# Performance work log

Measured on AMD Instinct MI355X. Metric: run time of the kernel, lower is better.

## Reference

```python
import jax, jax.numpy as jnp
import numpy as np

E, B, T, DIN, D = 8, 16, 512, 256, 256  # ensemble, batch, seq, input_dim, d_model*factor


def setup_inputs() -> dict:
    key = jax.random.key(0)
    ks = jax.random.split(key, 9)
    s_in = 1.0 / np.sqrt(DIN)
    s_d = 1.0 / np.sqrt(D)
    return {
        "x": jax.random.normal(ks[0], (E, B, T, DIN), jnp.float32),
        "hidden": jnp.zeros((1, E * B, 2 * D), jnp.float32),
        "rnn_start": (jax.random.uniform(ks[1], (B, T, 1)) < 0.02).astype(jnp.float32),
        "W_in": jax.random.normal(ks[2], (2, E, DIN, D), jnp.float32) * s_in,
        "b_in": jax.random.normal(ks[3], (2, E, D), jnp.float32) * 0.01,
        "W_mid": jax.random.normal(ks[4], (4, E, D, D), jnp.float32) * s_d,
        "b_mid": jax.random.normal(ks[5], (4, E, D), jnp.float32) * 0.01,
        "W_out": jax.random.normal(ks[6], (E, D, D), jnp.float32) * s_d,
        "b_out": jax.random.normal(ks[7], (E, D), jnp.float32) * 0.01,
    }


def _scan_tie_input_gate(v, f, h0):
    # h_t = f_t * h_{t-1} + (1 - f_t) * v_t  (tied input gate), via associative scan.
    # v, f: [N, T, D]; h0: [N, 1, D]
    b = (1.0 - f) * v

    def combine(x, y):
        a1, b1 = x
        a2, b2 = y
        return a1 * a2, a2 * b1 + b2

    A, Bc = jax.lax.associative_scan(combine, (f, b), axis=1)
    out = A * h0 + Bc  # [N, T, D]
    return out, out[:, -1:, :]


def reference(x, hidden, rnn_start, W_in, b_in, W_mid, b_mid, W_out, b_out):
    # --- first GILR stage ---
    u = jnp.einsum('ebti,meio->mebto', x, W_in) + b_in[:, :, None, None, :]
    v = jnp.tanh(u[0])
    f = jax.nn.sigmoid(u[1])
    f = f * (1.0 - rnn_start)[None]  # rnn_start [B,T,1] broadcasts over E, D

    vr = v.reshape(E * B, T, D)
    fr = f.reshape(E * B, T, D)

    h_pre, h_mid = jnp.split(hidden, 2, axis=-1)          # each [1, E*B, D]
    h_pre = jnp.transpose(h_pre, (1, 0, 2))               # [E*B, 1, D]
    h_mid = jnp.transpose(h_mid, (1, 0, 2))

    vr, h_pre_last = _scan_tie_input_gate(vr, fr, h_pre)
    v4 = vr.reshape(E, B, T, D)

    # --- LSTM-like middle stage ---
    u = jnp.einsum('ebti,meio->mebto', v4, W_mid) + b_mid[:, :, None, None, :]
    f = jax.nn.sigmoid(u[0])
    i = jax.nn.sigmoid(u[1])
    o = jax.nn.sigmoid(u[2])
    z = jnp.tanh(u[3])
    f = f * (1.0 - rnn_start)[None]

    fr = f.reshape(E * B, T, D)
    izr = (i * z).reshape(E * B, T, D)
    orr = o.reshape(E * B, T, D)

    out, h_mid_last = _scan_tie_input_gate(izr, fr, h_mid)
    out = out * orr
    out4 = out.reshape(E, B, T, D)

    # --- output projection ---
    out4 = jnp.einsum('ebti,eio->ebto', out4, W_out) + b_out[:, None, None, :]

    hidden_out = jnp.transpose(jnp.concatenate([h_pre_last, h_mid_last], axis=-1), (1, 0, 2))
    return out4, hidden_out
```

## Files before the change

kernel.cpp:

```cpp
#include <hip/hip_runtime.h>
#include <hip/hip_bf16.h>
#include <stdint.h>
#include <stddef.h>


typedef __bf16 bf16x8 __attribute__((ext_vector_type(8)));
typedef __bf16 bf16x4 __attribute__((ext_vector_type(4)));
typedef __bf16 bf16x2 __attribute__((ext_vector_type(2)));
typedef float  f32x4  __attribute__((ext_vector_type(4)));
typedef float  f32x2  __attribute__((ext_vector_type(2)));

#define E_ 8
#define M_ 8192
#define K_ 256

__device__ __forceinline__ float sigm_f(float x) {
    return __builtin_amdgcn_rcpf(1.0f + __expf(-x));
}
__device__ __forceinline__ float tanh_f(float x) {
    return 1.0f - 2.0f * __builtin_amdgcn_rcpf(1.0f + __expf(2.0f * x));
}

__device__ __forceinline__ void g2lds16(const void* g, void* l) {
    __builtin_amdgcn_global_load_lds((const __attribute__((address_space(1))) void*)g,
                                     (__attribute__((address_space(3))) void*)l, 16, 0, 0);
}

template <int D>
__device__ __forceinline__ float dppshr(float x) {
    return __builtin_bit_cast(float,
        __builtin_amdgcn_update_dpp(0, __builtin_bit_cast(int, x),
                                    0x110 | D, 0xF, 0xF, true));
}

__device__ __forceinline__ void lane_scan(float& A, float& B, float& EA, float& EB, int ln15) {
    float As, Bs;
    Bs = dppshr<1>(B); As = dppshr<1>(A); B = __builtin_fmaf(A, Bs, B); A = (ln15 >= 1) ? A * As : A;
    Bs = dppshr<2>(B); As = dppshr<2>(A); B = __builtin_fmaf(A, Bs, B); A = (ln15 >= 2) ? A * As : A;
    Bs = dppshr<4>(B); As = dppshr<4>(A); B = __builtin_fmaf(A, Bs, B); A = (ln15 >= 4) ? A * As : A;
    Bs = dppshr<8>(B); As = dppshr<8>(A); B = __builtin_fmaf(A, Bs, B); A = (ln15 >= 8) ? A * As : A;
    EA = dppshr<1>(A); EA = (ln15 >= 1) ? EA : 1.0f;
    EB = dppshr<1>(B);
}

__global__ __launch_bounds__(256) void convx_k(const float* __restrict__ x, __bf16* __restrict__ xb) {
    int i = blockIdx.x * 256 + threadIdx.x;
    float4 v = ((const float4*)x)[i];
    bf16x4 o;
    o[0] = (__bf16)v.x; o[1] = (__bf16)v.y; o[2] = (__bf16)v.z; o[3] = (__bf16)v.w;
    ((bf16x4*)xb)[i] = o;
}

__global__ __launch_bounds__(256) void transw_k(const float* __restrict__ src, __bf16* __restrict__ dst,
                                                int NG, int ilv) {
    int ge = blockIdx.z;
    int g = ge >> 3, e = ge & 7;
    int k0 = blockIdx.x * 64, d0 = blockIdx.y * 64;
    __shared__ float tile[64][65];
    int t = threadIdx.x;
#pragma unroll
    for (int j = 0; j < 16; ++j) {
        int lin = j * 256 + t;
        int r = lin >> 6, c = lin & 63;
        tile[r][c] = src[((size_t)(ge * 256 + k0 + r)) * 256 + d0 + c];
    }
    __syncthreads();
#pragma unroll
    for (int j = 0; j < 16; ++j) {
        int lin = j * 256 + t;
        int r = lin >> 6, c = lin & 63;
        int d = d0 + r;
        int row = ilv ? (d * NG + g) : (g * 256 + d);
        dst[((size_t)(e * NG * 256 + row)) * K_ + k0 + c] = (__bf16)tile[c][r];
    }
}

template <int MODE, int NG>
__global__ __launch_bounds__(512, 1) void gemm_k(const __bf16* __restrict__ A,
                                                 const __bf16* __restrict__ Wt,
                                                 const float* __restrict__ bias,
                                                 const float* __restrict__ rs,
                                                 __bf16* __restrict__ gout,
                                                 float* __restrict__ fout,
                                                 const float* __restrict__ hidden,
                                                 float* __restrict__ hidout) {
    constexpr int NT  = NG * 2;
    constexpr int NMT = 2 * NT;
    const int tid = threadIdx.x;
    const int bid = blockIdx.x;
    const int e  = bid & 7;
    const int rr = bid >> 3;
    const int nt = rr & (NT - 1);
    const int ms = rr / NT;
    const int mt0 = ms * NMT;
    const int lane = tid & 63, wid = tid >> 6;
    const int wr = wid >> 2, wc = wid & 3;
    const int ln15 = lane & 15, ln16 = lane >> 4;

    __shared__ __align__(16) __bf16 As[2][32768];
    __shared__ float cAl[64], cBl[64];
    __shared__ float chL[2][64];

    bf16x8 Breg[2][8];
    {
        const __bf16* bp = Wt + ((size_t)e * (NG * 256) + nt * 128 + wc * 32 + ln15) * K_ + ln16 * 8;
#pragma unroll
        for (int j = 0; j < 2; ++j)
#pragma unroll
            for (int s = 0; s < 8; ++s)
                Breg[j][s] = *(const bf16x8*)(bp + (size_t)j * 16 * K_ + s * 32);
    }
    f32x4 bias_v[2];
#pragma unroll
    for (int j = 0; j < 2; ++j) {
        int n0 = nt * 128 + wc * 32 + j * 16 + (ln16 << 2);
        if constexpr (MODE == 0) {
#pragma unroll
            for (int q = 0; q < 4; ++q) {
                int n = n0 + q;
                bias_v[j][q] = bias[((n & 1) * E_ + e) * 256 + (n >> 1)];
            }
        } else if constexpr (MODE == 1) {
#pragma unroll
            for (int q = 0; q < 4; ++q) {
                int n = n0 + q;
                bias_v[j][q] = bias[((n & 3) * E_ + e) * 256 + (n >> 2)];
            }
        } else {
            bias_v[j] = *(const f32x4*)&bias[e * 256 + n0];
        }
    }

    const size_t Ae = ((size_t)e * M_ + (size_t)mt0 * 128) * K_;
    const int sr = tid >> 5, sr2 = sr >> 2;
    const int gg0 = (tid & 31) ^ sr2;
    const __bf16* sE = A + Ae + (size_t)sr * K_ + gg0 * 8;
    const __bf16* sO = A + Ae + (size_t)sr * K_ + (gg0 ^ 4) * 8;
    __bf16* const dbase0 = &As[0][tid * 8];
    __bf16* const dbase1 = &As[1][tid * 8];

    auto stage = [&](int tt, int buf) {
        __bf16* d = buf ? dbase1 : dbase0;
        const size_t toff = (size_t)tt * (128 * K_);
#pragma unroll
        for (int q = 0; q < 8; ++q)
            g2lds16(((q & 1) ? sO : sE) + toff + q * (16 * K_), d + q * 4096);
    };

    const int rowb = (wr * 64 + ln15 * 4) * K_;
    const int gb = ln16 ^ (lane & 7);
    const int pe_off = rowb + gb * 8;
    const int po_off = rowb + (gb ^ 4) * 8;

    auto compute = [&](f32x4 (&acc)[4][2], int buf) {
        const __bf16* pe = &As[0][0] + buf * 32768 + pe_off;
        const __bf16* po = &As[0][0] + buf * 32768 + po_off;
#pragma unroll
        for (int s = 0; s < 8; ++s) {
            const __bf16* p = (s & 1) ? po : pe;
            bf16x8 af[4];
#pragma unroll
            for (int i = 0; i < 4; ++i)
                af[i] = *(const bf16x8*)(p + i * K_ + (s >> 1) * 64);
#pragma unroll
            for (int i = 0; i < 4; ++i)
#pragma unroll
                for (int j = 0; j < 2; ++j)
                    acc[i][j] = __builtin_amdgcn_mfma_f32_16x16x32_bf16(Breg[j][s], af[i], acc[i][j], 0, 0, 0);
        }
    };

    stage(0, 0);
    asm volatile("s_waitcnt vmcnt(0)" ::: "memory");
    __builtin_amdgcn_s_barrier();
    __builtin_amdgcn_sched_barrier(0);

    if constexpr (MODE == 2) {
        f32x4 acc[4][2] = {};
        int buf = 0;
        for (int t = 0; t < NMT; ++t) {
            if (t + 1 < NMT) stage(t + 1, buf ^ 1);
            compute(acc, buf);
            const int mb = (mt0 + t) * 128 + wr * 64 + ln15 * 4;
#pragma unroll
            for (int j = 0; j < 2; ++j) {
                const int n0 = nt * 128 + wc * 32 + j * 16 + (ln16 << 2);
#pragma unroll
                for (int i = 0; i < 4; ++i) {
                    f32x4 o = acc[i][j] + bias_v[j];
                    *(f32x4*)&fout[((size_t)e * M_ + mb + i) * 256 + n0] = o;
                    acc[i][j] = f32x4{};
                }
            }
            asm volatile("s_waitcnt vmcnt(8) lgkmcnt(0)" ::: "memory");
            __builtin_amdgcn_s_barrier();
            __builtin_amdgcn_sched_barrier(0);
            buf ^= 1;
        }
        return;
    } else {
        auto do_epi = [&](f32x4 (&acc)[4][2], int tp, const f32x4& rs4p, const float* hidvp) {
            const bool cs = ((tp & 3) == 0);
            const int c = tp >> 2;
            const int mb = (mt0 + tp) * 128 + wr * 64 + ln15 * 4;
            f32x4 rsv;
#pragma unroll
            for (int q = 0; q < 4; ++q) rsv[q] = 1.0f - rs4p[q];

            if constexpr (MODE == 1) {
                float PA[2][4], PB[2][4], Ov[2][4], LA[2], LB[2], EA[2], EB[2];
#pragma unroll
                for (int j = 0; j < 2; ++j) {
#pragma unroll
                    for (int i = 0; i < 4; ++i) {
                        float f  = sigm_f(acc[i][j][0] + bias_v[j][0]) * rsv[i];
                        float iv = sigm_f(acc[i][j][1] + bias_v[j][1]);
                        float o  = sigm_f(acc[i][j][2] + bias_v[j][2]);
                        float z  = tanh_f(acc[i][j][3] + bias_v[j][3]);
                        float b  = (1.0f - f) * iv * z;
                        Ov[j][i] = o;
                        if (i == 0) { PA[j][0] = f; PB[j][0] = b; }
                        else { PB[j][i] = __builtin_fmaf(f, PB[j][i - 1], b); PA[j][i] = PA[j][i - 1] * f; }
                        acc[i][j] = f32x4{};
                    }
                    LA[j] = PA[j][3]; LB[j] = PB[j][3];
                    lane_scan(LA[j], LB[j], EA[j], EB[j], ln15);
                }
                if (wr == 0 && ln15 == 15) {
#pragma unroll
                    for (int j = 0; j < 2; ++j) {
                        int sl = wc * 8 + j * 4 + ln16;
                        cAl[sl] = LA[j]; cBl[sl] = LB[j];
                    }
                }
                asm volatile("s_waitcnt lgkmcnt(0)" ::: "memory");
                __builtin_amdgcn_s_barrier();
#pragma unroll
                for (int j = 0; j < 2; ++j) {
                    const int sl = wc * 8 + j * 4 + ln16;
                    const int d = nt * 32 + wc * 8 + j * 4 + ln16;
                    float hp = cs ? hidvp[j] : chL[tp & 1][sl];
                    float hs = wr ? __builtin_fmaf(cAl[sl], hp, cBl[sl]) : hp;
                    float h0 = __builtin_fmaf(EA[j], hs, EB[j]);
#pragma unroll
                    for (int i = 0; i < 4; ++i) {
                        float h = __builtin_fmaf(PA[j][i], h0, PB[j][i]);
                        gout[((size_t)e * M_ + mb + i) * 256 + d] = (__bf16)(h * Ov[j][i]);
                    }
                    if (wr == 1 && ln15 == 15) {
                        float he = __builtin_fmaf(LA[j], hs, LB[j]);
                        chL[(tp + 1) & 1][sl] = he;
                        if ((tp & 3) == 3)
                            hidout[(e * 16 + ms * 4 + c) * 512 + 256 + d] = he;
                    }
                }
            } else {
                float PA[2][2][4], PB[2][2][4], LA[2][2], LB[2][2], EA[2][2], EB[2][2];
#pragma unroll
                for (int j = 0; j < 2; ++j) {
#pragma unroll
                    for (int dq = 0; dq < 2; ++dq) {
#pragma unroll
                        for (int i = 0; i < 4; ++i) {
                            float uv = acc[i][j][dq * 2 + 0] + bias_v[j][dq * 2 + 0];
                            float uf = acc[i][j][dq * 2 + 1] + bias_v[j][dq * 2 + 1];
                            float f = sigm_f(uf) * rsv[i];
                            float b = (1.0f - f) * tanh_f(uv);
                            if (i == 0) { PA[j][dq][0] = f; PB[j][dq][0] = b; }
                            else { PB[j][dq][i] = __builtin_fmaf(f, PB[j][dq][i - 1], b);
                                   PA[j][dq][i] = PA[j][dq][i - 1] * f; }
                        }
                        LA[j][dq] = PA[j][dq][3]; LB[j][dq] = PB[j][dq][3];
                        lane_scan(LA[j][dq], LB[j][dq], EA[j][dq], EB[j][dq], ln15);
                    }
#pragma unroll
                    for (int i = 0; i < 4; ++i) acc[i][j] = f32x4{};
                }
                if (wr == 0 && ln15 == 15) {
#pragma unroll
                    for (int j = 0; j < 2; ++j)
#pragma unroll
                        for (int dq = 0; dq < 2; ++dq) {
                            int sl = wc * 16 + j * 8 + ln16 * 2 + dq;
                            cAl[sl] = LA[j][dq]; cBl[sl] = LB[j][dq];
                        }
                }
                asm volatile("s_waitcnt lgkmcnt(0)" ::: "memory");
                __builtin_amdgcn_s_barrier();
#pragma unroll
                for (int j = 0; j < 2; ++j) {
                    const int D0 = nt * 64 + wc * 16 + j * 8 + ln16 * 2;
                    float h0q[2];
#pragma unroll
                    for (int dq = 0; dq < 2; ++dq) {
                        const int sl = wc * 16 + j * 8 + ln16 * 2 + dq;
                        float hp = cs ? hidvp[j * 2 + dq] : chL[tp & 1][sl];
                        float hs = wr ? __builtin_fmaf(cAl[sl], hp, cBl[sl]) : hp;
                        h0q[dq] = __builtin_fmaf(EA[j][dq], hs, EB[j][dq]);
                        if (wr == 1 && ln15 == 15) {
                            float he = __builtin_fmaf(LA[j][dq], hs, LB[j][dq]);
                            chL[(tp + 1) & 1][sl] = he;
                            if ((tp & 3) == 3)
                                hidout[(e * 16 + ms * 2 + c) * 512 + D0 + dq] = he;
                        }
                    }
#pragma unroll
                    for (int i = 0; i < 4; ++i) {
                        float ha = __builtin_fmaf(PA[j][0][i], h0q[0], PB[j][0][i]);
                        float hb = __builtin_fmaf(PA[j][1][i], h0q[1], PB[j][1][i]);
                        bf16x2 pk; pk[0] = (__bf16)ha; pk[1] = (__bf16)hb;
                        *(unsigned int*)&gout[((size_t)e * M_ + mb + i) * 256 + D0] =
                            __builtin_bit_cast(unsigned int, pk);
                    }
                }
            }
        };

        f32x4 accA[4][2] = {}, accB[4][2] = {};
        f32x4 rs4_p = {};
        float hidv_p[4] = {0.f, 0.f, 0.f, 0.f};
        int buf = 0;

        auto iter = [&](int t, f32x4 (&accC)[4][2], f32x4 (&accP)[4][2]) {
            const int c = t >> 2;
            f32x4 rs4_n;
            float hidv_n[4] = {0.f, 0.f, 0.f, 0.f};
            {
                const int mbh = (mt0 + t) * 128 + wr * 64 + ln15 * 4;
                rs4_n = *(const f32x4*)&rs[mbh];
                if constexpr (MODE == 1) {
                    const int nrow = e * 16 + ms * 4 + c;
                    hidv_n[0] = hidden[nrow * 512 + 256 + (nt * 32 + wc * 8 + 0 + ln16)];
                    hidv_n[1] = hidden[nrow * 512 + 256 + (nt * 32 + wc * 8 + 4 + ln16)];
                } else {
                    const int nrow = e * 16 + ms * 2 + c;
                    f32x2 ha = *(const f32x2*)&hidden[nrow * 512 + (nt * 64 + wc * 16 + 0 + ln16 * 2)];
                    f32x2 hb = *(const f32x2*)&hidden[nrow * 512 + (nt * 64 + wc * 16 + 8 + ln16 * 2)];
                    hidv_n[0] = ha[0]; hidv_n[1] = ha[1]; hidv_n[2] = hb[0]; hidv_n[3] = hb[1];
                }
                __builtin_amdgcn_sched_barrier(0);
            }
            if (t + 1 < NMT) stage(t + 1, buf ^ 1);
            compute(accC, buf);
            if (t > 0) do_epi(accP, t - 1, rs4_p, hidv_p);
            if (t == 0) {
                asm volatile("s_waitcnt vmcnt(0) lgkmcnt(0)" ::: "memory");
            } else {
                asm volatile("s_waitcnt vmcnt(8) lgkmcnt(0)" ::: "memory");
            }
            __builtin_amdgcn_s_barrier();
            __builtin_amdgcn_sched_barrier(0);
            buf ^= 1;
            rs4_p = rs4_n;
#pragma unroll
            for (int q = 0; q < 4; ++q) hidv_p[q] = hidv_n[q];
        };

#pragma unroll 1
        for (int t2 = 0; t2 < NMT; t2 += 2) {
            iter(t2, accA, accB);
            iter(t2 + 1, accB, accA);
        }
        do_epi(accB, NMT - 1, rs4_p, hidv_p);
    }
}

extern "C" void kernel_launch(void* const* d_in, const int* in_sizes, int n_in,
                              void* d_out, int out_size, void* d_ws, size_t ws_size,
                              hipStream_t stream) {
    const float* x      = (const float*)d_in[0];
    const float* hidden = (const float*)d_in[1];
    const float* rs     = (const float*)d_in[2];
    const float* W_in   = (const float*)d_in[3];
    const float* b_in   = (const float*)d_in[4];
    const float* W_mid  = (const float*)d_in[5];
    const float* b_mid  = (const float*)d_in[6];
    const float* W_out  = (const float*)d_in[7];
    const float* b_out  = (const float*)d_in[8];
    float* out = (float*)d_out;

    char* ws = (char*)d_ws;
    const size_t MiB = (size_t)1 << 20;
    __bf16* Wt1 = (__bf16*)(ws + 0);
    __bf16* Wt2 = (__bf16*)(ws + 2 * MiB);
    __bf16* Wt3 = (__bf16*)(ws + 6 * MiB);
    __bf16* v4b = (__bf16*)(ws + 8 * MiB);
    __bf16* xb  = (__bf16*)(ws + 40 * MiB);
    __bf16* G   = (__bf16*)(ws + 72 * MiB);

    float* hidout = out + (size_t)E_ * M_ * 256;

    convx_k<<<16384, 256, 0, stream>>>(x, xb);
    transw_k<<<dim3(4, 4, 16), 256, 0, stream>>>(W_in, Wt1, 2, 1);
    transw_k<<<dim3(4, 4, 32), 256, 0, stream>>>(W_mid, Wt2, 4, 1);
    transw_k<<<dim3(4, 4, 8), 256, 0, stream>>>(W_out, Wt3, 1, 0);

    gemm_k<0, 2><<<256, 512, 0, stream>>>(xb, Wt1, b_in, rs, v4b, nullptr, hidden, hidout);
    gemm_k<1, 4><<<256, 512, 0, stream>>>(v4b, Wt2, b_mid, rs, G, nullptr, hidden, hidout);
    gemm_k<2, 1><<<256, 512, 0, stream>>>(G, Wt3, b_out, nullptr, nullptr, out, nullptr, nullptr);
}
```

Baseline: 170.9 us.

## Fuse fp32-to-bf16 input conversion into first GEMM and merge weight transposes

Drops the standalone convx_k kernel. The first GEMM now loads fp32 x directly into registers, converts it to bf16, and writes it to LDS in a register-staged software pipeline. This removes the bf16 copy of x (a 32 MiB write plus its reread) and one launch. It also folds the three weight-transpose launches into a single launch. The cost is higher register pressure and twice the global bytes per tile in MODE 0, and the LDS write now happens after the wait for global loads rather than asynchronously.

```diff
diff --git a/kernel.cpp b/kernel.cpp
--- a/kernel.cpp
+++ b/kernel.cpp
@@ -43,17 +43,17 @@
     EB = dppshr<1>(B);
 }
 
-__global__ __launch_bounds__(256) void convx_k(const float* __restrict__ x, __bf16* __restrict__ xb) {
-    int i = blockIdx.x * 256 + threadIdx.x;
-    float4 v = ((const float4*)x)[i];
-    bf16x4 o;
-    o[0] = (__bf16)v.x; o[1] = (__bf16)v.y; o[2] = (__bf16)v.z; o[3] = (__bf16)v.w;
-    ((bf16x4*)xb)[i] = o;
-}
-
-__global__ __launch_bounds__(256) void transw_k(const float* __restrict__ src, __bf16* __restrict__ dst,
-                                                int NG, int ilv) {
-    int ge = blockIdx.z;
+__global__ __launch_bounds__(256) void transw_all(const float* __restrict__ W_in,
+                                                  const float* __restrict__ W_mid,
+                                                  const float* __restrict__ W_out,
+                                                  __bf16* __restrict__ Wt1,
+                                                  __bf16* __restrict__ Wt2,
+                                                  __bf16* __restrict__ Wt3) {
+    int z = blockIdx.z;
+    const float* src; __bf16* dst; int NG, ilv, ge;
+    if (z < 16)      { src = W_in;  dst = Wt1; NG = 2; ilv = 1; ge = z; }
+    else if (z < 48) { src = W_mid; dst = Wt2; NG = 4; ilv = 1; ge = z - 16; }
+    else             { src = W_out; dst = Wt3; NG = 1; ilv = 0; ge = z - 48; }
     int g = ge >> 3, e = ge & 7;
     int k0 = blockIdx.x * 64, d0 = blockIdx.y * 64;
     __shared__ float tile[64][65];
@@ -77,6 +77,7 @@
 
 template <int MODE, int NG>
 __global__ __launch_bounds__(512, 1) void gemm_k(const __bf16* __restrict__ A,
+                                                 const float* __restrict__ Af,
                                                  const __bf16* __restrict__ Wt,
                                                  const float* __restrict__ bias,
                                                  const float* __restrict__ rs,
@@ -131,11 +132,18 @@
         }
     }
 
-    const size_t Ae = ((size_t)e * M_ + (size_t)mt0 * 128) * K_;
     const int sr = tid >> 5, sr2 = sr >> 2;
     const int gg0 = (tid & 31) ^ sr2;
-    const __bf16* sE = A + Ae + (size_t)sr * K_ + gg0 * 8;
-    const __bf16* sO = A + Ae + (size_t)sr * K_ + (gg0 ^ 4) * 8;
+    const size_t Aoff = ((size_t)e * M_ + (size_t)mt0 * 128) * K_;
+    const __bf16* sE = nullptr; const __bf16* sO = nullptr;
+    const float*  sEf = nullptr; const float* sOf = nullptr;
+    if constexpr (MODE == 0) {
+        sEf = Af + Aoff + (size_t)sr * K_ + gg0 * 8;
+        sOf = Af + Aoff + (size_t)sr * K_ + (gg0 ^ 4) * 8;
+    } else {
+        sE = A + Aoff + (size_t)sr * K_ + gg0 * 8;
+        sO = A + Aoff + (size_t)sr * K_ + (gg0 ^ 4) * 8;
+    }
     __bf16* const dbase0 = &As[0][tid * 8];
     __bf16* const dbase1 = &As[1][tid * 8];
 
@@ -145,6 +153,27 @@
 #pragma unroll
         for (int q = 0; q < 8; ++q)
             g2lds16(((q & 1) ? sO : sE) + toff + q * (16 * K_), d + q * 4096);
+    };
+
+    f32x4 tA[8], tB[8];
+    auto loadx = [&](int tt) {
+        const size_t toff = (size_t)tt * (128 * K_);
+#pragma unroll
+        for (int q = 0; q < 8; ++q) {
+            const float* s = ((q & 1) ? sOf : sEf) + toff + q * (16 * K_);
+            tA[q] = *(const f32x4*)s;
+            tB[q] = *(const f32x4*)(s + 4);
+        }
+    };
+    auto writex = [&](int buf) {
+        __bf16* d = buf ? dbase1 : dbase0;
+#pragma unroll
+        for (int q = 0; q < 8; ++q) {
+            bf16x8 w;
+#pragma unroll
+            for (int k = 0; k < 4; ++k) { w[k] = (__bf16)tA[q][k]; w[4 + k] = (__bf16)tB[q][k]; }
+            *(bf16x8*)(d + q * 4096) = w;
+        }
     };
 
     const int rowb = (wr * 64 + ln15 * 4) * K_;
@@ -170,12 +199,11 @@
         }
     };
 
-    stage(0, 0);
-    asm volatile("s_waitcnt vmcnt(0)" ::: "memory");
-    __builtin_amdgcn_s_barrier();
-    __builtin_amdgcn_sched_barrier(0);
-
     if constexpr (MODE == 2) {
+        stage(0, 0);
+        asm volatile("s_waitcnt vmcnt(0)" ::: "memory");
+        __builtin_amdgcn_s_barrier();
+        __builtin_amdgcn_sched_barrier(0);
         f32x4 acc[4][2] = {};
         int buf = 0;
         for (int t = 0; t < NMT; ++t) {
@@ -315,6 +343,18 @@
                 }
             }
         };
+
+        if constexpr (MODE == 0) {
+            loadx(0);
+            asm volatile("s_waitcnt vmcnt(0)" ::: "memory");
+            writex(0);
+            asm volatile("s_waitcnt lgkmcnt(0)" ::: "memory");
+        } else {
+            stage(0, 0);
+            asm volatile("s_waitcnt vmcnt(0)" ::: "memory");
+        }
+        __builtin_amdgcn_s_barrier();
+        __builtin_amdgcn_sched_barrier(0);
 
         f32x4 accA[4][2] = {}, accB[4][2] = {};
         f32x4 rs4_p = {};
@@ -340,14 +380,23 @@
                 }
                 __builtin_amdgcn_sched_barrier(0);
             }
-            if (t + 1 < NMT) stage(t + 1, buf ^ 1);
+            if constexpr (MODE == 0) {
+                if (t + 1 < NMT) loadx(t + 1);
+                __builtin_amdgcn_sched_barrier(0);
+            } else {
+                if (t + 1 < NMT) stage(t + 1, buf ^ 1);
+            }
             compute(accC, buf);
             if (t > 0) do_epi(accP, t - 1, rs4_p, hidv_p);
             if (t == 0) {
-                asm volatile("s_waitcnt vmcnt(0) lgkmcnt(0)" ::: "memory");
+                asm volatile("s_waitcnt vmcnt(0)" ::: "memory");
             } else {
-                asm volatile("s_waitcnt vmcnt(8) lgkmcnt(0)" ::: "memory");
-            }
+                asm volatile("s_waitcnt vmcnt(8)" ::: "memory");
+            }
+            if constexpr (MODE == 0) {
+                if (t + 1 < NMT) writex(buf ^ 1);
+            }
+            asm volatile("s_waitcnt lgkmcnt(0)" ::: "memory");
             __builtin_amdgcn_s_barrier();
             __builtin_amdgcn_sched_barrier(0);
             buf ^= 1;
@@ -385,17 +434,13 @@
     __bf16* Wt2 = (__bf16*)(ws + 2 * MiB);
     __bf16* Wt3 = (__bf16*)(ws + 6 * MiB);
     __bf16* v4b = (__bf16*)(ws + 8 * MiB);
-    __bf16* xb  = (__bf16*)(ws + 40 * MiB);
     __bf16* G   = (__bf16*)(ws + 72 * MiB);
 
     float* hidout = out + (size_t)E_ * M_ * 256;
 
-    convx_k<<<16384, 256, 0, stream>>>(x, xb);
-    transw_k<<<dim3(4, 4, 16), 256, 0, stream>>>(W_in, Wt1, 2, 1);
-    transw_k<<<dim3(4, 4, 32), 256, 0, stream>>>(W_mid, Wt2, 4, 1);
-    transw_k<<<dim3(4, 4, 8), 256, 0, stream>>>(W_out, Wt3, 1, 0);
-
-    gemm_k<0, 2><<<256, 512, 0, stream>>>(xb, Wt1, b_in, rs, v4b, nullptr, hidden, hidout);
-    gemm_k<1, 4><<<256, 512, 0, stream>>>(v4b, Wt2, b_mid, rs, G, nullptr, hidden, hidout);
-    gemm_k<2, 1><<<256, 512, 0, stream>>>(G, Wt3, b_out, nullptr, nullptr, out, nullptr, nullptr);
-}
+    transw_all<<<dim3(4, 4, 56), 256, 0, stream>>>(W_in, W_mid, W_out, Wt1, Wt2, Wt3);
+
+    gemm_k<0, 2><<<256, 512, 0, stream>>>(nullptr, x, Wt1, b_in, rs, v4b, nullptr, hidden, hidout);
+    gemm_k<1, 4><<<256, 512, 0, stream>>>(v4b, nullptr, Wt2, b_mid, rs, G, nullptr, hidden, hidout);
+    gemm_k<2, 1><<<256, 512, 0, stream>>>(G, nullptr, Wt3, b_out, nullptr, nullptr, out, nullptr, nullptr);
+}
```

Result: faster. 162.3 us (-5.0%).
